# Performance work log

Measured on AMD Instinct MI355X. Metric: run time of the kernel, lower is better.

The kernel has to match this reference:

```python
import jax, jax.numpy as jnp
import numpy as np
import math

BATCH, CLS, ATT_DIM, IMG_DIM = 256, 500, 1024, 1024
ATT_HC, HIDDEN_C = 256, 1024
T_TEMP = 10.0
DEGREE = 30
THRESH = math.cos(math.pi * DEGREE / 180.0)
NEG = -9.0e15


def setup_inputs() -> dict:
    key = jax.random.key(0)
    ks = jax.random.split(key, 9)
    inp = {
        "image_feats": jax.random.normal(ks[0], (BATCH, IMG_DIM), dtype=jnp.float32),
        "attributes": jax.random.normal(ks[1], (CLS, ATT_DIM), dtype=jnp.float32),
        "unused": 0,
        # learned parameters (kaiming-like scaling)
        "att_g": jax.random.normal(ks[2], (ATT_DIM, ATT_HC), dtype=jnp.float32) / math.sqrt(ATT_DIM),
        "img_w": jax.random.normal(ks[3], (IMG_DIM, HIDDEN_C), dtype=jnp.float32) / math.sqrt(IMG_DIM),
        "sem_w": jax.random.normal(ks[4], (ATT_DIM, HIDDEN_C), dtype=jnp.float32) / math.sqrt(ATT_DIM),
        "sem_b": jax.random.normal(ks[5], (1, HIDDEN_C), dtype=jnp.float32) / math.sqrt(IMG_DIM),
        "fc_w": jax.random.normal(ks[6], (1, HIDDEN_C), dtype=jnp.float32) / math.sqrt(HIDDEN_C),
        "fc_b": jax.random.normal(ks[7], (1,), dtype=jnp.float32) / math.sqrt(HIDDEN_C),
    }
    return inp


def _get_new_attribute(attributes, att_g):
    # project attributes, cosine similarity between all class pairs
    g = attributes @ att_g                                    # [cls, att_hC]
    gn = g / jnp.linalg.norm(g, axis=1, keepdims=True)        # row-normalize
    sim = gn @ gn.T                                           # [cls, cls] cosine sims
    raw = jnp.where(sim > THRESH, sim, NEG)                   # angular-threshold mask
    attention = jax.nn.softmax(raw * T_TEMP, axis=1)          # [cls, cls]
    return attention @ attributes                             # [cls, att_dim]


def reference(image_feats, attributes, unused, att_g, img_w, sem_w, sem_b, fc_w, fc_b):
    att_outs = _get_new_attribute(attributes, att_g)          # [cls, att_dim]
    # factor the broadcast: identical math to matmul on expanded tensors
    img_h = image_feats @ img_w                               # [batch, hidden]
    sem_h = att_outs @ sem_w                                  # [cls, hidden]
    hidden = jax.nn.relu(img_h[:, None, :] + sem_h[None, :, :] + sem_b[None, :, :])  # [batch, cls, hidden]
    out = jnp.einsum('bch,h->bc', hidden, fc_w[0]) + fc_b[0]  # [batch, cls]
    return out
```

## Files before the change

### kernel.cpp

```cpp
#include <hip/hip_runtime.h>
#include <math.h>

#define BATCH 256
#define CLS 500
#define T_TEMP_ 10.0f
#define THRESH_ 0.86602540378443864676f
#define NEGV -9.0e15f

typedef __attribute__((ext_vector_type(8))) short short8;
typedef __attribute__((ext_vector_type(8))) unsigned short u16x8;
typedef __attribute__((ext_vector_type(4))) unsigned short u16x4;
typedef __attribute__((ext_vector_type(4))) float f32x4;
typedef __attribute__((ext_vector_type(2))) float f32x2;

static __device__ __forceinline__ unsigned short f2bf(float x) {
    unsigned int u = __builtin_bit_cast(unsigned int, x);
    u += 0x7fff + ((u >> 16) & 1);
    return (unsigned short)(u >> 16);
}
static __device__ __forceinline__ float bf2f(unsigned short v) {
    return __builtin_bit_cast(float, (unsigned int)v << 16);
}
static __device__ __forceinline__ float fel(const float4& v, int j) { return (&v.x)[j]; }
static __device__ __forceinline__ u16x8 pack8(const float4& a, const float4& b) {
    u16x8 o;
    o[0] = f2bf(a.x); o[1] = f2bf(a.y); o[2] = f2bf(a.z); o[3] = f2bf(a.w);
    o[4] = f2bf(b.x); o[5] = f2bf(b.y); o[6] = f2bf(b.z); o[7] = f2bf(b.w);
    return o;
}

__global__ __launch_bounds__(256) void gpart_kernel(
    const float* __restrict__ attrs, const float* __restrict__ attg,
    float* __restrict__ gpart)
{
    __shared__ unsigned short As[64][40];
    __shared__ unsigned short Bs[128][40];
    const int t = threadIdx.x;
    const int bid = blockIdx.x;
    const int mt = bid >> 4, nt = (bid >> 3) & 1, split = bid & 7;
    const int n0 = nt * 128, ar0 = mt * 64, k0 = split * 128;

    const int w = t >> 6, lane = t & 63;
    const int wr = w >> 1, wc = w & 1;
    const int fr = lane & 15, kg = lane >> 4;
    const int as_row = t >> 2, as_kq = t & 3;
    const int bs_nc = (t & 31) * 4, bs_kr = t >> 5;

    f32x4 acc[2][4];
    #pragma unroll
    for (int i = 0; i < 2; ++i)
        #pragma unroll
        for (int j = 0; j < 4; ++j) acc[i][j] = (f32x4){0.f, 0.f, 0.f, 0.f};

    for (int kb = k0; kb < k0 + 128; kb += 32) {
        {
            const int gr = ar0 + as_row;
            float4 v0 = make_float4(0.f,0.f,0.f,0.f), v1 = v0;
            if (gr < CLS) {
                const float* ap = &attrs[(size_t)gr * 1024 + kb + as_kq * 8];
                v0 = *(const float4*)ap; v1 = *(const float4*)(ap + 4);
            }
            *(u16x8*)&As[as_row][as_kq * 8] = pack8(v0, v1);
        }
        {
            const float* bp = &attg[(size_t)(kb + bs_kr * 4) * 256 + n0 + bs_nc];
            float4 r0 = *(const float4*)(bp);
            float4 r1 = *(const float4*)(bp + 256);
            float4 r2 = *(const float4*)(bp + 512);
            float4 r3 = *(const float4*)(bp + 768);
            #pragma unroll
            for (int j = 0; j < 4; ++j) {
                unsigned int lo = (unsigned int)f2bf(fel(r0, j)) | ((unsigned int)f2bf(fel(r1, j)) << 16);
                unsigned int hi = (unsigned int)f2bf(fel(r2, j)) | ((unsigned int)f2bf(fel(r3, j)) << 16);
                uint2 u2; u2.x = lo; u2.y = hi;
                *(uint2*)&Bs[bs_nc + j][bs_kr * 4] = u2;
            }
        }
        __syncthreads();
        short8 af[2], bfr[4];
        #pragma unroll
        for (int i = 0; i < 2; ++i) af[i] = *(short8*)&As[wr * 32 + i * 16 + fr][kg * 8];
        #pragma unroll
        for (int j = 0; j < 4; ++j) bfr[j] = *(short8*)&Bs[wc * 64 + j * 16 + fr][kg * 8];
        #pragma unroll
        for (int i = 0; i < 2; ++i)
            #pragma unroll
            for (int j = 0; j < 4; ++j)
                acc[i][j] = __builtin_amdgcn_mfma_f32_16x16x32_bf16(af[i], bfr[j], acc[i][j], 0, 0, 0);
        __syncthreads();
    }

    float* Gp = gpart + (size_t)split * (512 * 256);
    const int orow0 = ar0 + wr * 32, ocol0 = n0 + wc * 64;
    #pragma unroll
    for (int i = 0; i < 2; ++i) {
        const int r0 = orow0 + i * 16 + kg * 4;
        #pragma unroll
        for (int j = 0; j < 4; ++j) {
            const int cc = ocol0 + j * 16 + fr;
            #pragma unroll
            for (int r = 0; r < 4; ++r)
                Gp[(size_t)(r0 + r) * 256 + cc] = acc[i][j][r];
        }
    }
}

__global__ __launch_bounds__(256) void reduce_norm_kernel(
    const float* __restrict__ part, unsigned short* __restrict__ gn_bf)
{
    const int c = blockIdx.x, t = threadIdx.x;
    float v = 0.f;
    #pragma unroll
    for (int z = 0; z < 8; ++z) v += part[(size_t)z * (512 * 256) + c * 256 + t];
    float ss = v * v;
    #pragma unroll
    for (int off = 32; off >= 1; off >>= 1) ss += __shfl_down(ss, off);
    __shared__ float red[4];
    const int wave = t >> 6, lane = t & 63;
    if (lane == 0) red[wave] = ss;
    __syncthreads();
    const float tot = red[0] + red[1] + red[2] + red[3];
    const float rn  = 1.f / sqrtf(tot);
    gn_bf[c * 256 + t] = f2bf(v * rn);
}

__global__ __launch_bounds__(256) void mfma_gemm_bf(
    const unsigned short* __restrict__ A1, int alim1,
    const unsigned short* __restrict__ A2, int a2t0, int alim2,
    const unsigned short* __restrict__ B1, const unsigned short* __restrict__ B2,
    float* __restrict__ C, unsigned short* __restrict__ Cbf,
    int M, int N, int K, int klen)
{
    __shared__ unsigned short As[64][40];
    __shared__ unsigned short Bs[128][40];

    const int t  = threadIdx.x;
    const int bx = blockIdx.x;
    const int n0 = blockIdx.y * 128;
    const int k0 = blockIdx.z * klen;

    const unsigned short* A; const unsigned short* B; int ar0, alim;
    if (bx < a2t0) { A = A1; B = B1; ar0 = bx * 64;          alim = alim1; }
    else           { A = A2; B = B2; ar0 = (bx - a2t0) * 64; alim = alim2; }

    const int w = t >> 6, lane = t & 63;
    const int wr = w >> 1, wc = w & 1;
    const int fr = lane & 15, kg = lane >> 4;

    const int a_row = t >> 2, a_k = (t & 3) * 8;
    const int b_row = t >> 1, b_k = (t & 1) * 16;
    const int gra = ar0 + a_row;
    const int grb = n0 + b_row;
    const bool va = gra < alim;
    const bool vb = grb < N;
    const size_t abase = (size_t)gra * K + a_k;
    const size_t bbase = (size_t)grb * K + b_k;

    u16x8 zz = {0,0,0,0,0,0,0,0};
    u16x8 pa = zz, pb0 = zz, pb1 = zz;
    if (va) pa = *(const u16x8*)&A[abase + k0];
    if (vb) { pb0 = *(const u16x8*)&B[bbase + k0]; pb1 = *(const u16x8*)&B[bbase + k0 + 8]; }

    f32x4 acc[2][4];
    #pragma unroll
    for (int i = 0; i < 2; ++i)
        #pragma unroll
        for (int j = 0; j < 4; ++j) acc[i][j] = (f32x4){0.f, 0.f, 0.f, 0.f};

    for (int kb = k0; kb < k0 + klen; kb += 32) {
        *(u16x8*)&As[a_row][a_k] = pa;
        *(u16x8*)&Bs[b_row][b_k] = pb0;
        *(u16x8*)&Bs[b_row][b_k + 8] = pb1;
        __syncthreads();

        const int kn = kb + 32;
        if (kn < k0 + klen) {
            if (va) pa = *(const u16x8*)&A[abase + kn];
            if (vb) { pb0 = *(const u16x8*)&B[bbase + kn]; pb1 = *(const u16x8*)&B[bbase + kn + 8]; }
        }

        short8 af[2], bfr[4];
        #pragma unroll
        for (int i = 0; i < 2; ++i) af[i] = *(short8*)&As[wr * 32 + i * 16 + fr][kg * 8];
        #pragma unroll
        for (int j = 0; j < 4; ++j) bfr[j] = *(short8*)&Bs[wc * 64 + j * 16 + fr][kg * 8];
        #pragma unroll
        for (int i = 0; i < 2; ++i)
            #pragma unroll
            for (int j = 0; j < 4; ++j)
                acc[i][j] = __builtin_amdgcn_mfma_f32_16x16x32_bf16(af[i], bfr[j], acc[i][j], 0, 0, 0);
        __syncthreads();
    }

    const int orow0 = bx * 64 + wr * 32, ocol0 = n0 + wc * 64;
    if (Cbf) {
        unsigned short* Cw = Cbf + (size_t)blockIdx.z * M * N;
        #pragma unroll
        for (int i = 0; i < 2; ++i) {
            const int r0 = orow0 + i * 16 + kg * 4;
            #pragma unroll
            for (int j = 0; j < 4; ++j) {
                const int cc = ocol0 + j * 16 + fr;
                if (cc >= N) continue;
                #pragma unroll
                for (int r = 0; r < 4; ++r) {
                    const int rr = r0 + r;
                    if (rr < M) Cw[(size_t)rr * N + cc] = f2bf(acc[i][j][r]);
                }
            }
        }
    } else {
        float* Cw = C + (gridDim.z > 1 ? (size_t)blockIdx.z * M * N : 0);
        #pragma unroll
        for (int i = 0; i < 2; ++i) {
            const int r0 = orow0 + i * 16 + kg * 4;
            #pragma unroll
            for (int j = 0; j < 4; ++j) {
                const int cc = ocol0 + j * 16 + fr;
                if (cc >= N) continue;
                #pragma unroll
                for (int r = 0; r < 4; ++r) {
                    const int rr = r0 + r;
                    if (rr < M) Cw[(size_t)rr * N + cc] = acc[i][j][r];
                }
            }
        }
    }
}

__global__ __launch_bounds__(256) void softmax_att_kernel(
    const float* __restrict__ sim, const float* __restrict__ attrs,
    unsigned short* __restrict__ att_outs)
{
    const int c = blockIdx.x, t = threadIdx.x;
    __shared__ float p_s[512];
    __shared__ float redm[4];
    __shared__ float reds[4];

    const float d0 = sim[(size_t)c * CLS + t];
    const float d1 = (t + 256 < CLS) ? sim[(size_t)c * CLS + t + 256] : NEGV;

    float vmax = fmaxf((d0 > THRESH_) ? d0 : NEGV, (d1 > THRESH_) ? d1 : NEGV);
    #pragma unroll
    for (int off = 32; off >= 1; off >>= 1) vmax = fmaxf(vmax, __shfl_down(vmax, off));
    const int wave = t >> 6, lane = t & 63;
    if (lane == 0) redm[wave] = vmax;
    __syncthreads();
    const float m = fmaxf(fmaxf(redm[0], redm[1]), fmaxf(redm[2], redm[3]));

    const float p0 = (d0 > THRESH_) ? expf(T_TEMP_ * (d0 - m)) : 0.f;
    const float p1 = (d1 > THRESH_) ? expf(T_TEMP_ * (d1 - m)) : 0.f;
    p_s[t] = p0;
    p_s[t + 256] = p1;
    float vsum = p0 + p1;
    #pragma unroll
    for (int off = 32; off >= 1; off >>= 1) vsum += __shfl_down(vsum, off);
    if (lane == 0) reds[wave] = vsum;
    __syncthreads();
    const float inv = 1.f / (reds[0] + reds[1] + reds[2] + reds[3]);

    float acc[4] = {0.f, 0.f, 0.f, 0.f};
    for (int base = 0; base < 512; base += 64) {
        const float pv_l = p_s[base + lane];
        unsigned long long mask = __ballot(pv_l > 0.f);
        while (mask) {
            const int l = __ffsll((long long)mask) - 1;
            mask &= mask - 1;
            const int c2 = base + l;
            const float pv = p_s[c2];
            const float* ar = &attrs[(size_t)c2 * 1024 + t];
            #pragma unroll
            for (int j = 0; j < 4; ++j) acc[j] += pv * ar[256 * j];
        }
    }
    #pragma unroll
    for (int j = 0; j < 4; ++j)
        att_outs[(size_t)c * 1024 + t + 256 * j] = f2bf(acc[j] * inv);
}

__global__ __launch_bounds__(256) void hid_kernel(
    const float* __restrict__ imgf, const unsigned short* __restrict__ atto_bf,
    const float* __restrict__ imgw, const float* __restrict__ semw,
    unsigned short* __restrict__ hidP)
{
    __shared__ unsigned short As[64][40];
    __shared__ unsigned short Bs[128][40];
    const int t = threadIdx.x;
    const int mt = blockIdx.x, nt = blockIdx.y, split = blockIdx.z;
    const int n0 = nt * 128, k0 = split * 512;
    const bool img_side = (mt < 4);
    const int ar0 = img_side ? mt * 64 : (mt - 4) * 64;
    const int alim = img_side ? 256 : 500;
    const float* Bf = img_side ? imgw : semw;

    const int w = t >> 6, lane = t & 63;
    const int wr = w >> 1, wc = w & 1;
    const int fr = lane & 15, kg = lane >> 4;
    const int as_row = t >> 2, as_kq = t & 3;
    const int bs_nc = (t & 31) * 4, bs_kr = t >> 5;

    f32x4 acc[2][4];
    #pragma unroll
    for (int i = 0; i < 2; ++i)
        #pragma unroll
        for (int j = 0; j < 4; ++j) acc[i][j] = (f32x4){0.f, 0.f, 0.f, 0.f};

    for (int kb = k0; kb < k0 + 512; kb += 32) {
        {
            const int gr = ar0 + as_row;
            if (img_side) {
                float4 v0 = make_float4(0.f,0.f,0.f,0.f), v1 = v0;
                if (gr < alim) {
                    const float* ap = &imgf[(size_t)gr * 1024 + kb + as_kq * 8];
                    v0 = *(const float4*)ap; v1 = *(const float4*)(ap + 4);
                }
                *(u16x8*)&As[as_row][as_kq * 8] = pack8(v0, v1);
            } else {
                u16x8 pa = {0,0,0,0,0,0,0,0};
                if (gr < alim) pa = *(const u16x8*)&atto_bf[(size_t)gr * 1024 + kb + as_kq * 8];
                *(u16x8*)&As[as_row][as_kq * 8] = pa;
            }
        }
        {
            const float* bp = &Bf[(size_t)(kb + bs_kr * 4) * 1024 + n0 + bs_nc];
            float4 r0 = *(const float4*)(bp);
            float4 r1 = *(const float4*)(bp + 1024);
            float4 r2 = *(const float4*)(bp + 2048);
            float4 r3 = *(const float4*)(bp + 3072);
            #pragma unroll
            for (int j = 0; j < 4; ++j) {
                unsigned int lo = (unsigned int)f2bf(fel(r0, j)) | ((unsigned int)f2bf(fel(r1, j)) << 16);
                unsigned int hi = (unsigned int)f2bf(fel(r2, j)) | ((unsigned int)f2bf(fel(r3, j)) << 16);
                uint2 u2; u2.x = lo; u2.y = hi;
                *(uint2*)&Bs[bs_nc + j][bs_kr * 4] = u2;
            }
        }
        __syncthreads();
        short8 af[2], bfr[4];
        #pragma unroll
        for (int i = 0; i < 2; ++i) af[i] = *(short8*)&As[wr * 32 + i * 16 + fr][kg * 8];
        #pragma unroll
        for (int j = 0; j < 4; ++j) bfr[j] = *(short8*)&Bs[wc * 64 + j * 16 + fr][kg * 8];
        #pragma unroll
        for (int i = 0; i < 2; ++i)
            #pragma unroll
            for (int j = 0; j < 4; ++j)
                acc[i][j] = __builtin_amdgcn_mfma_f32_16x16x32_bf16(af[i], bfr[j], acc[i][j], 0, 0, 0);
        __syncthreads();
    }

    unsigned short* Cw = hidP + (size_t)split * (756 * 1024);
    const int orow0 = mt * 64 + wr * 32, ocol0 = n0 + wc * 64;
    #pragma unroll
    for (int i = 0; i < 2; ++i) {
        const int r0 = orow0 + i * 16 + kg * 4;
        #pragma unroll
        for (int j = 0; j < 4; ++j) {
            const int cc = ocol0 + j * 16 + fr;
            #pragma unroll
            for (int r = 0; r < 4; ++r) {
                const int rr = r0 + r;
                if (rr < 756) Cw[(size_t)rr * 1024 + cc] = f2bf(acc[i][j][r]);
            }
        }
    }
}

__global__ __launch_bounds__(256) void fused_out_partial(
    const unsigned short* __restrict__ part, const float* __restrict__ sem_b,
    const float* __restrict__ fc_w, float* __restrict__ outpart)
{
    __shared__ float imgs[64][68];
    __shared__ float sems[64][68];
    __shared__ float fcs[128];

    const size_t pstride = (size_t)756 * 1024;
    const int t  = threadIdx.x;
    const int tb = t >> 4, tc = t & 15;
    const int b0 = blockIdx.x * 64, c0 = blockIdx.y * 64;
    const int h0 = blockIdx.z * 128;

    if (t < 32) *(float4*)&fcs[t * 4] = *(const float4*)&fc_w[h0 + t * 4];

    f32x2 acc2[4][4];
    #pragma unroll
    for (int i = 0; i < 4; ++i)
        #pragma unroll
        for (int j = 0; j < 4; ++j) acc2[i][j] = (f32x2){0.f, 0.f};

    for (int hs = 0; hs < 2; ++hs) {
        const int hb = h0 + hs * 64;
        #pragma unroll
        for (int i = 0; i < 4; ++i) {
            const int row = (t >> 4) + 16 * i;
            const int col = (t & 15) * 4;
            f32x4 iv = {0.f, 0.f, 0.f, 0.f};
            const unsigned short* pi = &part[(size_t)(b0 + row) * 1024 + hb + col];
            #pragma unroll
            for (int z = 0; z < 2; ++z) {
                u16x4 vz = *(const u16x4*)(pi + (size_t)z * pstride);
                iv[0] += bf2f(vz[0]); iv[1] += bf2f(vz[1]);
                iv[2] += bf2f(vz[2]); iv[3] += bf2f(vz[3]);
            }
            *(f32x4*)&imgs[row][col] = iv;

            f32x4 sv = {0.f, 0.f, 0.f, 0.f};
            if (c0 + row < CLS) {
                const unsigned short* ps2 = &part[(size_t)(256 + c0 + row) * 1024 + hb + col];
                #pragma unroll
                for (int z = 0; z < 2; ++z) {
                    u16x4 vz = *(const u16x4*)(ps2 + (size_t)z * pstride);
                    sv[0] += bf2f(vz[0]); sv[1] += bf2f(vz[1]);
                    sv[2] += bf2f(vz[2]); sv[3] += bf2f(vz[3]);
                }
                const f32x4 bb = *(const f32x4*)&sem_b[hb + col];
                sv += bb;
            }
            *(f32x4*)&sems[row][col] = sv;
        }
        __syncthreads();

        #pragma unroll
        for (int h4 = 0; h4 < 16; ++h4) {
            f32x4 ia[4], sa[4];
            #pragma unroll
            for (int i = 0; i < 4; ++i) ia[i] = *(f32x4*)&imgs[tb + 16 * i][h4 * 4];
            #pragma unroll
            for (int j = 0; j < 4; ++j) sa[j] = *(f32x4*)&sems[tc + 16 * j][h4 * 4];
            const f32x4 wv = *(const f32x4*)&fcs[hs * 64 + h4 * 4];
            #pragma unroll
            for (int e2 = 0; e2 < 2; ++e2) {
                const f32x2 w2 = {wv[2 * e2], wv[2 * e2 + 1]};
                f32x2 ia2[4], sa2[4];
                #pragma unroll
                for (int i = 0; i < 4; ++i) ia2[i] = (f32x2){ia[i][2 * e2], ia[i][2 * e2 + 1]};
                #pragma unroll
                for (int j = 0; j < 4; ++j) sa2[j] = (f32x2){sa[j][2 * e2], sa[j][2 * e2 + 1]};
                #pragma unroll
                for (int i = 0; i < 4; ++i)
                    #pragma unroll
                    for (int j = 0; j < 4; ++j) {
                        f32x2 s = ia2[i] + sa2[j];
                        s = __builtin_elementwise_max(s, (f32x2){0.f, 0.f});
                        acc2[i][j] += s * w2;
                    }
            }
        }
        __syncthreads();
    }

    const int nh = blockIdx.z;
    #pragma unroll
    for (int i = 0; i < 4; ++i) {
        const int b = b0 + tb + 16 * i;
        #pragma unroll
        for (int j = 0; j < 4; ++j) {
            const int cc = c0 + tc + 16 * j;
            if (cc < CLS)
                outpart[((size_t)nh * BATCH + b) * CLS + cc] = acc2[i][j][0] + acc2[i][j][1];
        }
    }
}

__global__ __launch_bounds__(256) void finalize_kernel(
    const float* __restrict__ partial, const float* __restrict__ fc_b,
    float* __restrict__ out)
{
    const int idx = blockIdx.x * 256 + threadIdx.x;
    if (idx >= BATCH * CLS) return;
    float s = fc_b[0];
    #pragma unroll
    for (int nh = 0; nh < 8; ++nh)
        s += partial[(size_t)nh * (BATCH * CLS) + idx];
    out[idx] = s;
}

extern "C" void kernel_launch(void* const* d_in, const int* in_sizes, int n_in,
                              void* d_out, int out_size, void* d_ws, size_t ws_size,
                              hipStream_t stream)
{
    const float* imgf  = (const float*)d_in[0];
    const float* attrs = (const float*)d_in[1];
    const float* attg  = (const float*)d_in[3];
    const float* imgw  = (const float*)d_in[4];
    const float* semw  = (const float*)d_in[5];
    const float* semb  = (const float*)d_in[6];
    const float* fcw   = (const float*)d_in[7];
    const float* fcb   = (const float*)d_in[8];
    float* out = (float*)d_out;

    char* ws = (char*)d_ws;
    size_t off = 0;
    auto alloc = [&](size_t b) { size_t o = off; off = (off + b + 255) & ~(size_t)255; return o; };
    float* gpart          = (float*)(ws + alloc((size_t)8 * 512 * 256 * 4));
    unsigned short* gn_bf = (unsigned short*)(ws + alloc((size_t)500 * 256 * 2));
    float* sim            = (float*)(ws + alloc((size_t)CLS * CLS * 4));
    unsigned short* atto  = (unsigned short*)(ws + alloc((size_t)500 * 1024 * 2));
    unsigned short* hidP  = (unsigned short*)(ws + alloc((size_t)2 * 756 * 1024 * 2));
    float* outP           = (float*)(ws + alloc((size_t)8 * BATCH * CLS * 4));

    gpart_kernel<<<128, 256, 0, stream>>>(attrs, attg, gpart);
    reduce_norm_kernel<<<CLS, 256, 0, stream>>>(gpart, gn_bf);
    mfma_gemm_bf<<<dim3(8, 4, 1), 256, 0, stream>>>(
        gn_bf, 500, gn_bf, 1000, 500, gn_bf, gn_bf,
        sim, nullptr, 500, 500, 256, 256);
    softmax_att_kernel<<<CLS, 256, 0, stream>>>(sim, attrs, atto);
    hid_kernel<<<dim3(12, 8, 2), 256, 0, stream>>>(imgf, atto, imgw, semw, hidP);
    fused_out_partial<<<dim3(4, 8, 8), 256, 0, stream>>>(hidP, semb, fcw, outP);
    finalize_kernel<<<(BATCH * CLS + 255) / 256, 256, 0, stream>>>(outP, fcb, out);
}
```

Baseline: 68.54 us.

## Reassociate attention through sem projection and merge GEMMs into one launch

Uses associativity, (attention@attrs)@sem_w = attention@(attrs@sem_w), so the sem-side GEMM runs on the raw attributes. That lets it share one launch with the attribute projection GEMM. The softmax is recomputed inside the fused output kernel as a sparse list of up to CAP neighbours per class, which gathers and weights precomputed sem_h rows. This removes the softmax_att and separate hid kernels and the atto buffer. In exchange, each fused block repeats the per-row softmax work, and rows with more than CAP neighbours take a slow fallback path.

```diff
diff --git a/kernel.cpp b/kernel.cpp
--- a/kernel.cpp
+++ b/kernel.cpp
@@ -6,6 +6,7 @@
 #define T_TEMP_ 10.0f
 #define THRESH_ 0.86602540378443864676f
 #define NEGV -9.0e15f
+#define CAP 16
 
 typedef __attribute__((ext_vector_type(8))) short short8;
 typedef __attribute__((ext_vector_type(8))) unsigned short u16x8;
@@ -29,16 +30,16 @@
     return o;
 }
 
-__global__ __launch_bounds__(256) void gpart_kernel(
+__global__ __launch_bounds__(256) void ka_kernel(
     const float* __restrict__ attrs, const float* __restrict__ attg,
-    float* __restrict__ gpart)
+    const float* __restrict__ imgf, const float* __restrict__ imgw,
+    const float* __restrict__ semw,
+    float* __restrict__ gpart, unsigned short* __restrict__ hid0)
 {
     __shared__ unsigned short As[64][40];
     __shared__ unsigned short Bs[128][40];
     const int t = threadIdx.x;
     const int bid = blockIdx.x;
-    const int mt = bid >> 4, nt = (bid >> 3) & 1, split = bid & 7;
-    const int n0 = nt * 128, ar0 = mt * 64, k0 = split * 128;
 
     const int w = t >> 6, lane = t & 63;
     const int wr = w >> 1, wc = w & 1;
@@ -52,55 +53,123 @@
         #pragma unroll
         for (int j = 0; j < 4; ++j) acc[i][j] = (f32x4){0.f, 0.f, 0.f, 0.f};
 
-    for (int kb = k0; kb < k0 + 128; kb += 32) {
-        {
-            const int gr = ar0 + as_row;
-            float4 v0 = make_float4(0.f,0.f,0.f,0.f), v1 = v0;
-            if (gr < CLS) {
-                const float* ap = &attrs[(size_t)gr * 1024 + kb + as_kq * 8];
-                v0 = *(const float4*)ap; v1 = *(const float4*)(ap + 4);
-            }
-            *(u16x8*)&As[as_row][as_kq * 8] = pack8(v0, v1);
-        }
-        {
-            const float* bp = &attg[(size_t)(kb + bs_kr * 4) * 256 + n0 + bs_nc];
-            float4 r0 = *(const float4*)(bp);
-            float4 r1 = *(const float4*)(bp + 256);
-            float4 r2 = *(const float4*)(bp + 512);
-            float4 r3 = *(const float4*)(bp + 768);
+    if (bid < 128) {
+        const int mt = bid >> 4, nt = (bid >> 3) & 1, split = bid & 7;
+        const int n0 = nt * 128, ar0 = mt * 64, k0 = split * 128;
+
+        for (int kb = k0; kb < k0 + 128; kb += 32) {
+            {
+                const int gr = ar0 + as_row;
+                float4 v0 = make_float4(0.f,0.f,0.f,0.f), v1 = v0;
+                if (gr < CLS) {
+                    const float* ap = &attrs[(size_t)gr * 1024 + kb + as_kq * 8];
+                    v0 = *(const float4*)ap; v1 = *(const float4*)(ap + 4);
+                }
+                *(u16x8*)&As[as_row][as_kq * 8] = pack8(v0, v1);
+            }
+            {
+                const float* bp = &attg[(size_t)(kb + bs_kr * 4) * 256 + n0 + bs_nc];
+                float4 r0 = *(const float4*)(bp);
+                float4 r1 = *(const float4*)(bp + 256);
+                float4 r2 = *(const float4*)(bp + 512);
+                float4 r3 = *(const float4*)(bp + 768);
+                #pragma unroll
+                for (int j = 0; j < 4; ++j) {
+                    unsigned int lo = (unsigned int)f2bf(fel(r0, j)) | ((unsigned int)f2bf(fel(r1, j)) << 16);
+                    unsigned int hi = (unsigned int)f2bf(fel(r2, j)) | ((unsigned int)f2bf(fel(r3, j)) << 16);
+                    uint2 u2; u2.x = lo; u2.y = hi;
+                    *(uint2*)&Bs[bs_nc + j][bs_kr * 4] = u2;
+                }
+            }
+            __syncthreads();
+            short8 af[2], bfr[4];
+            #pragma unroll
+            for (int i = 0; i < 2; ++i) af[i] = *(short8*)&As[wr * 32 + i * 16 + fr][kg * 8];
+            #pragma unroll
+            for (int j = 0; j < 4; ++j) bfr[j] = *(short8*)&Bs[wc * 64 + j * 16 + fr][kg * 8];
+            #pragma unroll
+            for (int i = 0; i < 2; ++i)
+                #pragma unroll
+                for (int j = 0; j < 4; ++j)
+                    acc[i][j] = __builtin_amdgcn_mfma_f32_16x16x32_bf16(af[i], bfr[j], acc[i][j], 0, 0, 0);
+            __syncthreads();
+        }
+
+        float* Gp = gpart + (size_t)split * (512 * 256);
+        const int orow0 = ar0 + wr * 32, ocol0 = n0 + wc * 64;
+        #pragma unroll
+        for (int i = 0; i < 2; ++i) {
+            const int r0 = orow0 + i * 16 + kg * 4;
             #pragma unroll
             for (int j = 0; j < 4; ++j) {
-                unsigned int lo = (unsigned int)f2bf(fel(r0, j)) | ((unsigned int)f2bf(fel(r1, j)) << 16);
-                unsigned int hi = (unsigned int)f2bf(fel(r2, j)) | ((unsigned int)f2bf(fel(r3, j)) << 16);
-                uint2 u2; u2.x = lo; u2.y = hi;
-                *(uint2*)&Bs[bs_nc + j][bs_kr * 4] = u2;
-            }
-        }
-        __syncthreads();
-        short8 af[2], bfr[4];
-        #pragma unroll
-        for (int i = 0; i < 2; ++i) af[i] = *(short8*)&As[wr * 32 + i * 16 + fr][kg * 8];
-        #pragma unroll
-        for (int j = 0; j < 4; ++j) bfr[j] = *(short8*)&Bs[wc * 64 + j * 16 + fr][kg * 8];
-        #pragma unroll
-        for (int i = 0; i < 2; ++i)
-            #pragma unroll
-            for (int j = 0; j < 4; ++j)
-                acc[i][j] = __builtin_amdgcn_mfma_f32_16x16x32_bf16(af[i], bfr[j], acc[i][j], 0, 0, 0);
-        __syncthreads();
-    }
-
-    float* Gp = gpart + (size_t)split * (512 * 256);
-    const int orow0 = ar0 + wr * 32, ocol0 = n0 + wc * 64;
-    #pragma unroll
-    for (int i = 0; i < 2; ++i) {
-        const int r0 = orow0 + i * 16 + kg * 4;
-        #pragma unroll
-        for (int j = 0; j < 4; ++j) {
-            const int cc = ocol0 + j * 16 + fr;
-            #pragma unroll
-            for (int r = 0; r < 4; ++r)
-                Gp[(size_t)(r0 + r) * 256 + cc] = acc[i][j][r];
+                const int cc = ocol0 + j * 16 + fr;
+                #pragma unroll
+                for (int r = 0; r < 4; ++r)
+                    Gp[(size_t)(r0 + r) * 256 + cc] = acc[i][j][r];
+            }
+        }
+    } else {
+        const int idx = bid - 128;
+        const int split = idx & 1, nt = (idx >> 1) & 7, mt = idx >> 4;
+        const int n0 = nt * 128, k0 = split * 512;
+        const bool img_side = (mt < 4);
+        const float* Af = img_side ? imgf : attrs;
+        const int ar0 = img_side ? mt * 64 : (mt - 4) * 64;
+        const int alim = img_side ? 256 : 500;
+        const float* Bf = img_side ? imgw : semw;
+
+        for (int kb = k0; kb < k0 + 512; kb += 32) {
+            {
+                const int gr = ar0 + as_row;
+                float4 v0 = make_float4(0.f,0.f,0.f,0.f), v1 = v0;
+                if (gr < alim) {
+                    const float* ap = &Af[(size_t)gr * 1024 + kb + as_kq * 8];
+                    v0 = *(const float4*)ap; v1 = *(const float4*)(ap + 4);
+                }
+                *(u16x8*)&As[as_row][as_kq * 8] = pack8(v0, v1);
+            }
+            {
+                const float* bp = &Bf[(size_t)(kb + bs_kr * 4) * 1024 + n0 + bs_nc];
+                float4 r0 = *(const float4*)(bp);
+                float4 r1 = *(const float4*)(bp + 1024);
+                float4 r2 = *(const float4*)(bp + 2048);
+                float4 r3 = *(const float4*)(bp + 3072);
+                #pragma unroll
+                for (int j = 0; j < 4; ++j) {
+                    unsigned int lo = (unsigned int)f2bf(fel(r0, j)) | ((unsigned int)f2bf(fel(r1, j)) << 16);
+                    unsigned int hi = (unsigned int)f2bf(fel(r2, j)) | ((unsigned int)f2bf(fel(r3, j)) << 16);
+                    uint2 u2; u2.x = lo; u2.y = hi;
+                    *(uint2*)&Bs[bs_nc + j][bs_kr * 4] = u2;
+                }
+            }
+            __syncthreads();
+            short8 af[2], bfr[4];
+            #pragma unroll
+            for (int i = 0; i < 2; ++i) af[i] = *(short8*)&As[wr * 32 + i * 16 + fr][kg * 8];
+            #pragma unroll
+            for (int j = 0; j < 4; ++j) bfr[j] = *(short8*)&Bs[wc * 64 + j * 16 + fr][kg * 8];
+            #pragma unroll
+            for (int i = 0; i < 2; ++i)
+                #pragma unroll
+                for (int j = 0; j < 4; ++j)
+                    acc[i][j] = __builtin_amdgcn_mfma_f32_16x16x32_bf16(af[i], bfr[j], acc[i][j], 0, 0, 0);
+            __syncthreads();
+        }
+
+        unsigned short* Cw = hid0 + (size_t)split * (756 * 1024);
+        const int orow0 = mt * 64 + wr * 32, ocol0 = n0 + wc * 64;
+        #pragma unroll
+        for (int i = 0; i < 2; ++i) {
+            const int r0 = orow0 + i * 16 + kg * 4;
+            #pragma unroll
+            for (int j = 0; j < 4; ++j) {
+                const int cc = ocol0 + j * 16 + fr;
+                #pragma unroll
+                for (int r = 0; r < 4; ++r) {
+                    const int rr = r0 + r;
+                    if (rr < 756) Cw[(size_t)rr * 1024 + cc] = f2bf(acc[i][j][r]);
+                }
+            }
         }
     }
 }
@@ -124,42 +193,31 @@
     gn_bf[c * 256 + t] = f2bf(v * rn);
 }
 
-__global__ __launch_bounds__(256) void mfma_gemm_bf(
-    const unsigned short* __restrict__ A1, int alim1,
-    const unsigned short* __restrict__ A2, int a2t0, int alim2,
-    const unsigned short* __restrict__ B1, const unsigned short* __restrict__ B2,
-    float* __restrict__ C, unsigned short* __restrict__ Cbf,
-    int M, int N, int K, int klen)
+__global__ __launch_bounds__(256) void sim_kernel(
+    const unsigned short* __restrict__ gn, float* __restrict__ S)
 {
     __shared__ unsigned short As[64][40];
     __shared__ unsigned short Bs[128][40];
-
     const int t  = threadIdx.x;
-    const int bx = blockIdx.x;
     const int n0 = blockIdx.y * 128;
-    const int k0 = blockIdx.z * klen;
-
-    const unsigned short* A; const unsigned short* B; int ar0, alim;
-    if (bx < a2t0) { A = A1; B = B1; ar0 = bx * 64;          alim = alim1; }
-    else           { A = A2; B = B2; ar0 = (bx - a2t0) * 64; alim = alim2; }
+    const int ar0 = blockIdx.x * 64;
 
     const int w = t >> 6, lane = t & 63;
     const int wr = w >> 1, wc = w & 1;
     const int fr = lane & 15, kg = lane >> 4;
-
     const int a_row = t >> 2, a_k = (t & 3) * 8;
     const int b_row = t >> 1, b_k = (t & 1) * 16;
     const int gra = ar0 + a_row;
     const int grb = n0 + b_row;
-    const bool va = gra < alim;
-    const bool vb = grb < N;
-    const size_t abase = (size_t)gra * K + a_k;
-    const size_t bbase = (size_t)grb * K + b_k;
+    const bool va = gra < CLS;
+    const bool vb = grb < CLS;
+    const size_t abase = (size_t)gra * 256 + a_k;
+    const size_t bbase = (size_t)grb * 256 + b_k;
 
     u16x8 zz = {0,0,0,0,0,0,0,0};
     u16x8 pa = zz, pb0 = zz, pb1 = zz;
-    if (va) pa = *(const u16x8*)&A[abase + k0];
-    if (vb) { pb0 = *(const u16x8*)&B[bbase + k0]; pb1 = *(const u16x8*)&B[bbase + k0 + 8]; }
+    if (va) pa = *(const u16x8*)&gn[abase];
+    if (vb) { pb0 = *(const u16x8*)&gn[bbase]; pb1 = *(const u16x8*)&gn[bbase + 8]; }
 
     f32x4 acc[2][4];
     #pragma unroll
@@ -167,16 +225,16 @@
         #pragma unroll
         for (int j = 0; j < 4; ++j) acc[i][j] = (f32x4){0.f, 0.f, 0.f, 0.f};
 
-    for (int kb = k0; kb < k0 + klen; kb += 32) {
+    for (int kb = 0; kb < 256; kb += 32) {
         *(u16x8*)&As[a_row][a_k] = pa;
         *(u16x8*)&Bs[b_row][b_k] = pb0;
         *(u16x8*)&Bs[b_row][b_k + 8] = pb1;
         __syncthreads();
 
         const int kn = kb + 32;
-        if (kn < k0 + klen) {
-            if (va) pa = *(const u16x8*)&A[abase + kn];
-            if (vb) { pb0 = *(const u16x8*)&B[bbase + kn]; pb1 = *(const u16x8*)&B[bbase + kn + 8]; }
+        if (kn < 256) {
+            if (va) pa = *(const u16x8*)&gn[abase + kn];
+            if (vb) { pb0 = *(const u16x8*)&gn[bbase + kn]; pb1 = *(const u16x8*)&gn[bbase + kn + 8]; }
         }
 
         short8 af[2], bfr[4];
@@ -192,195 +250,95 @@
         __syncthreads();
     }
 
-    const int orow0 = bx * 64 + wr * 32, ocol0 = n0 + wc * 64;
-    if (Cbf) {
-        unsigned short* Cw = Cbf + (size_t)blockIdx.z * M * N;
-        #pragma unroll
-        for (int i = 0; i < 2; ++i) {
-            const int r0 = orow0 + i * 16 + kg * 4;
-            #pragma unroll
-            for (int j = 0; j < 4; ++j) {
-                const int cc = ocol0 + j * 16 + fr;
-                if (cc >= N) continue;
-                #pragma unroll
-                for (int r = 0; r < 4; ++r) {
-                    const int rr = r0 + r;
-                    if (rr < M) Cw[(size_t)rr * N + cc] = f2bf(acc[i][j][r]);
-                }
-            }
-        }
-    } else {
-        float* Cw = C + (gridDim.z > 1 ? (size_t)blockIdx.z * M * N : 0);
-        #pragma unroll
-        for (int i = 0; i < 2; ++i) {
-            const int r0 = orow0 + i * 16 + kg * 4;
-            #pragma unroll
-            for (int j = 0; j < 4; ++j) {
-                const int cc = ocol0 + j * 16 + fr;
-                if (cc >= N) continue;
-                #pragma unroll
-                for (int r = 0; r < 4; ++r) {
-                    const int rr = r0 + r;
-                    if (rr < M) Cw[(size_t)rr * N + cc] = acc[i][j][r];
-                }
-            }
-        }
-    }
-}
-
-__global__ __launch_bounds__(256) void softmax_att_kernel(
-    const float* __restrict__ sim, const float* __restrict__ attrs,
-    unsigned short* __restrict__ att_outs)
-{
-    const int c = blockIdx.x, t = threadIdx.x;
-    __shared__ float p_s[512];
-    __shared__ float redm[4];
-    __shared__ float reds[4];
-
-    const float d0 = sim[(size_t)c * CLS + t];
-    const float d1 = (t + 256 < CLS) ? sim[(size_t)c * CLS + t + 256] : NEGV;
-
-    float vmax = fmaxf((d0 > THRESH_) ? d0 : NEGV, (d1 > THRESH_) ? d1 : NEGV);
-    #pragma unroll
-    for (int off = 32; off >= 1; off >>= 1) vmax = fmaxf(vmax, __shfl_down(vmax, off));
-    const int wave = t >> 6, lane = t & 63;
-    if (lane == 0) redm[wave] = vmax;
-    __syncthreads();
-    const float m = fmaxf(fmaxf(redm[0], redm[1]), fmaxf(redm[2], redm[3]));
-
-    const float p0 = (d0 > THRESH_) ? expf(T_TEMP_ * (d0 - m)) : 0.f;
-    const float p1 = (d1 > THRESH_) ? expf(T_TEMP_ * (d1 - m)) : 0.f;
-    p_s[t] = p0;
-    p_s[t + 256] = p1;
-    float vsum = p0 + p1;
-    #pragma unroll
-    for (int off = 32; off >= 1; off >>= 1) vsum += __shfl_down(vsum, off);
-    if (lane == 0) reds[wave] = vsum;
-    __syncthreads();
-    const float inv = 1.f / (reds[0] + reds[1] + reds[2] + reds[3]);
-
-    float acc[4] = {0.f, 0.f, 0.f, 0.f};
-    for (int base = 0; base < 512; base += 64) {
-        const float pv_l = p_s[base + lane];
-        unsigned long long mask = __ballot(pv_l > 0.f);
-        while (mask) {
-            const int l = __ffsll((long long)mask) - 1;
-            mask &= mask - 1;
-            const int c2 = base + l;
-            const float pv = p_s[c2];
-            const float* ar = &attrs[(size_t)c2 * 1024 + t];
-            #pragma unroll
-            for (int j = 0; j < 4; ++j) acc[j] += pv * ar[256 * j];
-        }
-    }
-    #pragma unroll
-    for (int j = 0; j < 4; ++j)
-        att_outs[(size_t)c * 1024 + t + 256 * j] = f2bf(acc[j] * inv);
-}
-
-__global__ __launch_bounds__(256) void hid_kernel(
-    const float* __restrict__ imgf, const unsigned short* __restrict__ atto_bf,
-    const float* __restrict__ imgw, const float* __restrict__ semw,
-    unsigned short* __restrict__ hidP)
-{
-    __shared__ unsigned short As[64][40];
-    __shared__ unsigned short Bs[128][40];
-    const int t = threadIdx.x;
-    const int mt = blockIdx.x, nt = blockIdx.y, split = blockIdx.z;
-    const int n0 = nt * 128, k0 = split * 512;
-    const bool img_side = (mt < 4);
-    const int ar0 = img_side ? mt * 64 : (mt - 4) * 64;
-    const int alim = img_side ? 256 : 500;
-    const float* Bf = img_side ? imgw : semw;
-
-    const int w = t >> 6, lane = t & 63;
-    const int wr = w >> 1, wc = w & 1;
-    const int fr = lane & 15, kg = lane >> 4;
-    const int as_row = t >> 2, as_kq = t & 3;
-    const int bs_nc = (t & 31) * 4, bs_kr = t >> 5;
-
-    f32x4 acc[2][4];
-    #pragma unroll
-    for (int i = 0; i < 2; ++i)
-        #pragma unroll
-        for (int j = 0; j < 4; ++j) acc[i][j] = (f32x4){0.f, 0.f, 0.f, 0.f};
-
-    for (int kb = k0; kb < k0 + 512; kb += 32) {
-        {
-            const int gr = ar0 + as_row;
-            if (img_side) {
-                float4 v0 = make_float4(0.f,0.f,0.f,0.f), v1 = v0;
-                if (gr < alim) {
-                    const float* ap = &imgf[(size_t)gr * 1024 + kb + as_kq * 8];
-                    v0 = *(const float4*)ap; v1 = *(const float4*)(ap + 4);
-                }
-                *(u16x8*)&As[as_row][as_kq * 8] = pack8(v0, v1);
-            } else {
-                u16x8 pa = {0,0,0,0,0,0,0,0};
-                if (gr < alim) pa = *(const u16x8*)&atto_bf[(size_t)gr * 1024 + kb + as_kq * 8];
-                *(u16x8*)&As[as_row][as_kq * 8] = pa;
-            }
-        }
-        {
-            const float* bp = &Bf[(size_t)(kb + bs_kr * 4) * 1024 + n0 + bs_nc];
-            float4 r0 = *(const float4*)(bp);
-            float4 r1 = *(const float4*)(bp + 1024);
-            float4 r2 = *(const float4*)(bp + 2048);
-            float4 r3 = *(const float4*)(bp + 3072);
-            #pragma unroll
-            for (int j = 0; j < 4; ++j) {
-                unsigned int lo = (unsigned int)f2bf(fel(r0, j)) | ((unsigned int)f2bf(fel(r1, j)) << 16);
-                unsigned int hi = (unsigned int)f2bf(fel(r2, j)) | ((unsigned int)f2bf(fel(r3, j)) << 16);
-                uint2 u2; u2.x = lo; u2.y = hi;
-                *(uint2*)&Bs[bs_nc + j][bs_kr * 4] = u2;
-            }
-        }
-        __syncthreads();
-        short8 af[2], bfr[4];
-        #pragma unroll
-        for (int i = 0; i < 2; ++i) af[i] = *(short8*)&As[wr * 32 + i * 16 + fr][kg * 8];
-        #pragma unroll
-        for (int j = 0; j < 4; ++j) bfr[j] = *(short8*)&Bs[wc * 64 + j * 16 + fr][kg * 8];
-        #pragma unroll
-        for (int i = 0; i < 2; ++i)
-            #pragma unroll
-            for (int j = 0; j < 4; ++j)
-                acc[i][j] = __builtin_amdgcn_mfma_f32_16x16x32_bf16(af[i], bfr[j], acc[i][j], 0, 0, 0);
-        __syncthreads();
-    }
-
-    unsigned short* Cw = hidP + (size_t)split * (756 * 1024);
-    const int orow0 = mt * 64 + wr * 32, ocol0 = n0 + wc * 64;
+    const int orow0 = ar0 + wr * 32, ocol0 = n0 + wc * 64;
     #pragma unroll
     for (int i = 0; i < 2; ++i) {
         const int r0 = orow0 + i * 16 + kg * 4;
         #pragma unroll
         for (int j = 0; j < 4; ++j) {
             const int cc = ocol0 + j * 16 + fr;
+            if (cc >= CLS) continue;
             #pragma unroll
             for (int r = 0; r < 4; ++r) {
                 const int rr = r0 + r;
-                if (rr < 756) Cw[(size_t)rr * 1024 + cc] = f2bf(acc[i][j][r]);
-            }
-        }
-    }
-}
-
-__global__ __launch_bounds__(256) void fused_out_partial(
-    const unsigned short* __restrict__ part, const float* __restrict__ sem_b,
-    const float* __restrict__ fc_w, float* __restrict__ outpart)
+                if (rr < CLS) S[(size_t)rr * CLS + cc] = acc[i][j][r];
+            }
+        }
+    }
+}
+
+__global__ __launch_bounds__(256) void fused_kernel(
+    const float* __restrict__ sim, const unsigned short* __restrict__ hid0,
+    const float* __restrict__ sem_b, const float* __restrict__ fc_w,
+    float* __restrict__ outpart)
 {
     __shared__ float imgs[64][68];
     __shared__ float sems[64][68];
     __shared__ float fcs[128];
+    __shared__ int   cnt_s[64];
+    __shared__ int   hitc2[64][CAP];
+    __shared__ float hitw[64][CAP];
+    __shared__ float mrow[64];
+    __shared__ float invrow[64];
 
     const size_t pstride = (size_t)756 * 1024;
     const int t  = threadIdx.x;
     const int tb = t >> 4, tc = t & 15;
     const int b0 = blockIdx.x * 64, c0 = blockIdx.y * 64;
     const int h0 = blockIdx.z * 128;
+    const int w = t >> 6, lane = t & 63;
 
     if (t < 32) *(float4*)&fcs[t * 4] = *(const float4*)&fc_w[h0 + t * 4];
+
+    for (int i = 0; i < 16; ++i) {
+        const int rl = w * 16 + i;
+        const int r  = c0 + rl;
+        float vals[8];
+        float vmax = NEGV;
+        if (r < CLS) {
+            #pragma unroll
+            for (int ch = 0; ch < 8; ++ch) {
+                const int c2 = ch * 64 + lane;
+                const float d = (c2 < CLS) ? sim[(size_t)r * CLS + c2] : NEGV;
+                vals[ch] = d;
+                vmax = fmaxf(vmax, (d > THRESH_) ? d : NEGV);
+            }
+        } else {
+            #pragma unroll
+            for (int ch = 0; ch < 8; ++ch) vals[ch] = NEGV;
+        }
+        #pragma unroll
+        for (int off = 32; off >= 1; off >>= 1) vmax = fmaxf(vmax, __shfl_down(vmax, off));
+        vmax = __shfl(vmax, 0);
+        float pvs[8];
+        float s = 0.f;
+        #pragma unroll
+        for (int ch = 0; ch < 8; ++ch) {
+            const float pv = (vals[ch] > THRESH_) ? expf(T_TEMP_ * (vals[ch] - vmax)) : 0.f;
+            pvs[ch] = pv; s += pv;
+        }
+        #pragma unroll
+        for (int off = 32; off >= 1; off >>= 1) s += __shfl_down(s, off);
+        s = __shfl(s, 0);
+        const float inv = (r < CLS) ? 1.f / s : 0.f;
+        int count = 0;
+        #pragma unroll
+        for (int ch = 0; ch < 8; ++ch) {
+            unsigned long long mk = __ballot(pvs[ch] > 0.f);
+            while (mk) {
+                const int l = __ffsll((long long)mk) - 1;
+                mk &= mk - 1;
+                const float wgt = __shfl(pvs[ch], l) * inv;
+                if (count < CAP && lane == 0) {
+                    hitc2[rl][count] = ch * 64 + l;
+                    hitw[rl][count]  = wgt;
+                }
+                ++count;
+            }
+        }
+        if (lane == 0) { cnt_s[rl] = count; mrow[rl] = vmax; invrow[rl] = inv; }
+    }
+    __syncthreads();
 
     f32x2 acc2[4][4];
     #pragma unroll
@@ -395,7 +353,7 @@
             const int row = (t >> 4) + 16 * i;
             const int col = (t & 15) * 4;
             f32x4 iv = {0.f, 0.f, 0.f, 0.f};
-            const unsigned short* pi = &part[(size_t)(b0 + row) * 1024 + hb + col];
+            const unsigned short* pi = &hid0[(size_t)(b0 + row) * 1024 + hb + col];
             #pragma unroll
             for (int z = 0; z < 2; ++z) {
                 u16x4 vz = *(const u16x4*)(pi + (size_t)z * pstride);
@@ -406,12 +364,39 @@
 
             f32x4 sv = {0.f, 0.f, 0.f, 0.f};
             if (c0 + row < CLS) {
-                const unsigned short* ps2 = &part[(size_t)(256 + c0 + row) * 1024 + hb + col];
-                #pragma unroll
-                for (int z = 0; z < 2; ++z) {
-                    u16x4 vz = *(const u16x4*)(ps2 + (size_t)z * pstride);
-                    sv[0] += bf2f(vz[0]); sv[1] += bf2f(vz[1]);
-                    sv[2] += bf2f(vz[2]); sv[3] += bf2f(vz[3]);
+                const int n = cnt_s[row];
+                if (n <= CAP) {
+                    for (int k = 0; k < n; ++k) {
+                        const int c2 = hitc2[row][k];
+                        const float wgt = hitw[row][k];
+                        const unsigned short* ps2 = &hid0[(size_t)(256 + c2) * 1024 + hb + col];
+                        f32x4 hv = {0.f, 0.f, 0.f, 0.f};
+                        #pragma unroll
+                        for (int z = 0; z < 2; ++z) {
+                            u16x4 vz = *(const u16x4*)(ps2 + (size_t)z * pstride);
+                            hv[0] += bf2f(vz[0]); hv[1] += bf2f(vz[1]);
+                            hv[2] += bf2f(vz[2]); hv[3] += bf2f(vz[3]);
+                        }
+                        sv += wgt * hv;
+                    }
+                } else {
+                    const int r = c0 + row;
+                    const float mr = mrow[row], ir = invrow[row];
+                    for (int c2 = 0; c2 < CLS; ++c2) {
+                        const float d = sim[(size_t)r * CLS + c2];
+                        if (d > THRESH_) {
+                            const float wgt = expf(T_TEMP_ * (d - mr)) * ir;
+                            const unsigned short* ps2 = &hid0[(size_t)(256 + c2) * 1024 + hb + col];
+                            f32x4 hv = {0.f, 0.f, 0.f, 0.f};
+                            #pragma unroll
+                            for (int z = 0; z < 2; ++z) {
+                                u16x4 vz = *(const u16x4*)(ps2 + (size_t)z * pstride);
+                                hv[0] += bf2f(vz[0]); hv[1] += bf2f(vz[1]);
+                                hv[2] += bf2f(vz[2]); hv[3] += bf2f(vz[3]);
+                            }
+                            sv += wgt * hv;
+                        }
+                    }
                 }
                 const f32x4 bb = *(const f32x4*)&sem_b[hb + col];
                 sv += bb;
@@ -440,9 +425,9 @@
                 for (int i = 0; i < 4; ++i)
                     #pragma unroll
                     for (int j = 0; j < 4; ++j) {
-                        f32x2 s = ia2[i] + sa2[j];
-                        s = __builtin_elementwise_max(s, (f32x2){0.f, 0.f});
-                        acc2[i][j] += s * w2;
+                        f32x2 s2 = ia2[i] + sa2[j];
+                        s2 = __builtin_elementwise_max(s2, (f32x2){0.f, 0.f});
+                        acc2[i][j] += s2 * w2;
                     }
             }
         }
@@ -495,17 +480,12 @@
     float* gpart          = (float*)(ws + alloc((size_t)8 * 512 * 256 * 4));
     unsigned short* gn_bf = (unsigned short*)(ws + alloc((size_t)500 * 256 * 2));
     float* sim            = (float*)(ws + alloc((size_t)CLS * CLS * 4));
-    unsigned short* atto  = (unsigned short*)(ws + alloc((size_t)500 * 1024 * 2));
-    unsigned short* hidP  = (unsigned short*)(ws + alloc((size_t)2 * 756 * 1024 * 2));
+    unsigned short* hid0  = (unsigned short*)(ws + alloc((size_t)2 * 756 * 1024 * 2));
     float* outP           = (float*)(ws + alloc((size_t)8 * BATCH * CLS * 4));
 
-    gpart_kernel<<<128, 256, 0, stream>>>(attrs, attg, gpart);
+    ka_kernel<<<320, 256, 0, stream>>>(attrs, attg, imgf, imgw, semw, gpart, hid0);
     reduce_norm_kernel<<<CLS, 256, 0, stream>>>(gpart, gn_bf);
-    mfma_gemm_bf<<<dim3(8, 4, 1), 256, 0, stream>>>(
-        gn_bf, 500, gn_bf, 1000, 500, gn_bf, gn_bf,
-        sim, nullptr, 500, 500, 256, 256);
-    softmax_att_kernel<<<CLS, 256, 0, stream>>>(sim, attrs, atto);
-    hid_kernel<<<dim3(12, 8, 2), 256, 0, stream>>>(imgf, atto, imgw, semw, hidP);
-    fused_out_partial<<<dim3(4, 8, 8), 256, 0, stream>>>(hidP, semb, fcw, outP);
+    sim_kernel<<<dim3(8, 4), 256, 0, stream>>>(gn_bf, sim);
+    fused_kernel<<<dim3(4, 8, 8), 256, 0, stream>>>(sim, hid0, semb, fcw, outP);
     finalize_kernel<<<(BATCH * CLS + 255) / 256, 256, 0, stream>>>(outP, fcb, out);
 }
```

Measured after the change: 80.57 us. 17.6% more time.
